# Performance work log

Measured on AMD Instinct MI355X. Metric: run time of the kernel, lower is better.

## Reference

```python
import jax, jax.numpy as jnp
import numpy as np

# Module constants (match init_kwargs)
H = 16            # num_heads
K = 64            # max_kernel_size
MAX_FREQ = 16.0
MIN_FREQ = 1.0
HALF_S = 16       # int(32**(1/1)) // 2
S = 2 * HALF_S + 1  # 33 sample offsets: -16..16
MAX_RECEPTIVE = HALF_S * MAX_FREQ  # 256.0


def setup_inputs() -> dict:
    key = jax.random.key(0)
    ks = jax.random.split(key, 6)
    B, L, C = 1, 4096, 1024
    x = jax.random.normal(ks[0], (B, L, C), dtype=jnp.float32)
    # Learned params (random small scale so offsets/kernels vary; torch inits
    # wave_proj to zeros but that degenerates the math under test).
    Ww = jax.random.normal(ks[1], (2 * H, C), dtype=jnp.float32) * 0.02
    bw = jnp.zeros((2 * H,), dtype=jnp.float32)
    Wk = jax.random.normal(ks[2], (H * K, C), dtype=jnp.float32) * 0.02
    bk = jnp.zeros((H * K,), dtype=jnp.float32)
    Wo = jax.random.normal(ks[3], (C, C), dtype=jnp.float32) * 0.02
    return {"x": x, "Ww": Ww, "bw": bw, "Wk": Wk, "bk": bk, "Wo": Wo}


def reference(x, Ww, bw, Wk, bk, Wo):
    B, L, C = x.shape
    D = C // H
    dt = x.dtype
    grid = jnp.arange(-HALF_S, HALF_S + 1, dtype=dt)  # (S,)

    # Predict per-position frequency / phase (averaged over heads)
    wp = jax.nn.silu(x @ Ww.T + bw).reshape(B, L, 2, H)
    freq = jax.nn.sigmoid(wp[:, :, 0]) * (MAX_FREQ - MIN_FREQ) + MIN_FREQ  # (B,L,H)
    phase = jnp.tanh(wp[:, :, 1]) * MAX_FREQ
    freq_avg = freq.mean(-1)    # (B,L)
    phase_avg = phase.mean(-1)  # (B,L)

    # Sample positions & gather indices
    rel_pos = grid[None, None, :] * freq_avg[..., None] + phase_avg[..., None]  # (B,L,S)
    centers = jnp.arange(L, dtype=dt)
    sample_pos = centers[None, :, None] + rel_pos                               # (B,L,S)
    valid = (sample_pos >= 0) & (sample_pos < L)
    sample_idx = jnp.clip(sample_pos.astype(jnp.int32), 0, L - 1)               # trunc toward 0, like torch .long()

    # Gather values: (B,L,S,C) -> (B,L,H,S,D)
    values = jax.vmap(lambda xf, idx: xf[idx])(x, sample_idx)
    values = values.reshape(B, L, S, H, D).transpose(0, 1, 3, 2, 4)

    # Kernel profile, linearly interpolated to sample positions
    kernel_max = jax.nn.silu(x @ Wk.T + bk).reshape(B, L, H, K)
    norm_pos = jnp.clip((rel_pos + MAX_RECEPTIVE) / (2.0 * MAX_RECEPTIVE), 0.0, 1.0)
    idx_float = norm_pos * (K - 1)                       # (B,L,S)
    idx_floor = jnp.clip(idx_float.astype(jnp.int32), 0, K - 2)
    w_ceil = (idx_float - idx_floor.astype(dt))[:, :, None, :]  # (B,L,1,S)
    w_floor = 1.0 - w_ceil
    ifl = jnp.broadcast_to(idx_floor[:, :, None, :], (B, L, H, S))
    k_floor = jnp.take_along_axis(kernel_max, ifl, axis=-1)
    k_ceil = jnp.take_along_axis(kernel_max, ifl + 1, axis=-1)
    kernel = (k_floor * w_floor + k_ceil * w_ceil) * valid[:, :, None, :].astype(dt)
    kernel = kernel / (kernel.sum(-1, keepdims=True) + 1e-8)

    out = jnp.einsum('blhsd,blhs->blhd', values, kernel).reshape(B, L, C)
    out = jax.nn.silu(out @ Wo.T)
    return out
```

## Files before the change

kernel.cpp:

```cpp
#include <hip/hip_runtime.h>
#include <math.h>

#define LDIM 4096
#define CDIM 1024
#define HDIM 16
#define KDIM 64
#define SDIM 33
#define HALF_SS 16
#define MAXF 16.0f
#define MINF 1.0f
#define MAXR 256.0f

__device__ __forceinline__ float sigmoid_np(float z) {
  float e = (float)exp(-(double)z);
  return __fdiv_rn(1.0f, __fadd_rn(1.0f, e));
}
__device__ __forceinline__ float silu_f(float z) {
  return __fmul_rn(z, sigmoid_np(z));
}

__device__ __forceinline__ float np_pairwise_sum(const float* a, int n) {
  float r[8];
#pragma unroll
  for (int j = 0; j < 8; ++j) r[j] = a[j];
  int i = 8;
  for (; i + 8 <= n; i += 8)
#pragma unroll
    for (int j = 0; j < 8; ++j) r[j] = __fadd_rn(r[j], a[i + j]);
  float res = __fadd_rn(__fadd_rn(__fadd_rn(r[0], r[1]), __fadd_rn(r[2], r[3])),
                        __fadd_rn(__fadd_rn(r[4], r[5]), __fadd_rn(r[6], r[7])));
  for (; i < n; ++i) res = __fadd_rn(res, a[i]);
  return res;
}

__global__ __launch_bounds__(256) void wave_kernel(
    const float* __restrict__ x, const float* __restrict__ Ww,
    const float* __restrict__ bw, float* __restrict__ fa, float* __restrict__ pa) {
  __shared__ float xs[CDIM];
  __shared__ float wp[2 * HDIM];
  int l = blockIdx.x;
  int tid = threadIdx.x;
  const float* xrow = x + (size_t)l * CDIM;
  for (int c = tid; c < CDIM; c += 256) xs[c] = xrow[c];
  __syncthreads();
  int j = tid >> 3, sub = tid & 7;
  const float* wrow = Ww + j * CDIM;
  double acc = 0.0;
  for (int c = sub; c < CDIM; c += 8) acc += (double)xs[c] * (double)wrow[c];
  for (int off = 4; off; off >>= 1) acc += __shfl_down(acc, off, 8);
  if (sub == 0) {
    float v32 = (float)(acc + (double)bw[j]);
    wp[j] = silu_f(v32);
  }
  __syncthreads();
  if (tid == 0) {
    float fv[HDIM], pv[HDIM];
    for (int h = 0; h < HDIM; ++h) {
      fv[h] = __fadd_rn(__fmul_rn(sigmoid_np(wp[h]), MAXF - MINF), MINF);
      float t32 = (float)tanh((double)wp[HDIM + h]);
      pv[h] = __fmul_rn(t32, MAXF);
    }
    fa[l] = __fdiv_rn(np_pairwise_sum(fv, HDIM), (float)HDIM);
    pa[l] = __fdiv_rn(np_pairwise_sum(pv, HDIM), (float)HDIM);
  }
}

__global__ __launch_bounds__(256) void gemm_bt_silu_f64(
    const float* __restrict__ A, const float* __restrict__ B,
    const float* __restrict__ bias, float* __restrict__ Cout,
    int M, int N, int Kd) {
  __shared__ double Asd[16][128];
  __shared__ double Bsd[16][64];
  int tid = threadIdx.x;
  int tx = tid & 15, ty = tid >> 4;
  int m0 = blockIdx.y * 128, n0 = blockIdx.x * 64;
  double acc[8][4] = {};
  for (int kt = 0; kt < Kd; kt += 16) {
#pragma unroll
    for (int q = 0; q < 2; ++q) {
      int e = tid + 256 * q;
      int row = e >> 2, kq = (e & 3) * 4;
      float4 va = *(const float4*)(A + (size_t)(m0 + row) * Kd + kt + kq);
      Asd[kq + 0][row] = (double)va.x; Asd[kq + 1][row] = (double)va.y;
      Asd[kq + 2][row] = (double)va.z; Asd[kq + 3][row] = (double)va.w;
    }
    {
      int row = tid >> 2, kq = (tid & 3) * 4;
      float4 vb = *(const float4*)(B + (size_t)(n0 + row) * Kd + kt + kq);
      Bsd[kq + 0][row] = (double)vb.x; Bsd[kq + 1][row] = (double)vb.y;
      Bsd[kq + 2][row] = (double)vb.z; Bsd[kq + 3][row] = (double)vb.w;
    }
    __syncthreads();
#pragma unroll
    for (int kk = 0; kk < 16; ++kk) {
      double a[8], b[4];
#pragma unroll
      for (int i = 0; i < 8; ++i) a[i] = Asd[kk][ty * 8 + i];
#pragma unroll
      for (int j2 = 0; j2 < 4; ++j2) b[j2] = Bsd[kk][tx * 4 + j2];
#pragma unroll
      for (int i = 0; i < 8; ++i)
#pragma unroll
        for (int j2 = 0; j2 < 4; ++j2) acc[i][j2] += a[i] * b[j2];
    }
    __syncthreads();
  }
#pragma unroll
  for (int i = 0; i < 8; ++i) {
    int mm = m0 + ty * 8 + i;
#pragma unroll
    for (int j2 = 0; j2 < 4; ++j2) {
      int nn = n0 + tx * 4 + j2;
      float v32 = (float)acc[i][j2];
      v32 = __fadd_rn(v32, bias[nn]);
      Cout[(size_t)mm * N + nn] = silu_f(v32);
    }
  }
}

__global__ __launch_bounds__(256) void gemm_bt_silu_f32(
    const float* __restrict__ A, const float* __restrict__ B,
    float* __restrict__ Cout, int M, int N, int Kd) {
  __shared__ float Asf[16][128];
  __shared__ float Bsf[16][128];
  int tid = threadIdx.x;
  int tx = tid & 15, ty = tid >> 4;
  int m0 = blockIdx.y * 128, n0 = blockIdx.x * 128;
  float acc[8][8] = {};
  for (int kt = 0; kt < Kd; kt += 16) {
#pragma unroll
    for (int q = 0; q < 2; ++q) {
      int e = tid + 256 * q;
      int row = e >> 2, kq = (e & 3) * 4;
      float4 va = *(const float4*)(A + (size_t)(m0 + row) * Kd + kt + kq);
      Asf[kq + 0][row] = va.x; Asf[kq + 1][row] = va.y;
      Asf[kq + 2][row] = va.z; Asf[kq + 3][row] = va.w;
      float4 vb = *(const float4*)(B + (size_t)(n0 + row) * Kd + kt + kq);
      Bsf[kq + 0][row] = vb.x; Bsf[kq + 1][row] = vb.y;
      Bsf[kq + 2][row] = vb.z; Bsf[kq + 3][row] = vb.w;
    }
    __syncthreads();
#pragma unroll
    for (int kk = 0; kk < 16; ++kk) {
      float4 a0 = *(const float4*)&Asf[kk][ty * 8];
      float4 a1 = *(const float4*)&Asf[kk][ty * 8 + 4];
      float4 b0 = *(const float4*)&Bsf[kk][tx * 8];
      float4 b1 = *(const float4*)&Bsf[kk][tx * 8 + 4];
      float a[8] = {a0.x, a0.y, a0.z, a0.w, a1.x, a1.y, a1.z, a1.w};
      float b[8] = {b0.x, b0.y, b0.z, b0.w, b1.x, b1.y, b1.z, b1.w};
#pragma unroll
      for (int i = 0; i < 8; ++i)
#pragma unroll
        for (int j2 = 0; j2 < 8; ++j2) acc[i][j2] += a[i] * b[j2];
    }
    __syncthreads();
  }
#pragma unroll
  for (int i = 0; i < 8; ++i) {
    int mm = m0 + ty * 8 + i;
#pragma unroll
    for (int j2 = 0; j2 < 8; ++j2) {
      int nn = n0 + tx * 8 + j2;
      Cout[(size_t)mm * N + nn] = silu_f(acc[i][j2]);
    }
  }
}

__global__ __launch_bounds__(256) void conv_kernel(
    const float* __restrict__ x, const float* __restrict__ km,
    const float* __restrict__ fa, const float* __restrict__ pa,
    float* __restrict__ conv) {
  int l = blockIdx.x;
  int tid = threadIdx.x;
  __shared__ int s_idx[SDIM];
  __shared__ int s_ifl[SDIM];
  __shared__ float s_wc[SDIM];
  __shared__ float s_val[SDIM];
  __shared__ float kern[HDIM][SDIM];
  __shared__ float s_den[HDIM];
  if (tid < SDIM) {
    float f = fa[l], p = pa[l];
    float rel = __fadd_rn(__fmul_rn((float)(tid - HALF_SS), f), p);
    float pos = __fadd_rn((float)l, rel);
    bool valid = (pos >= 0.f) && (pos < (float)LDIM);
    int idx = (int)pos;
    idx = min(max(idx, 0), LDIM - 1);
    s_idx[tid] = idx;
    s_val[tid] = valid ? 1.f : 0.f;
    float np_ = __fdiv_rn(__fadd_rn(rel, MAXR), 2.f * MAXR);
    np_ = fminf(fmaxf(np_, 0.f), 1.f);
    float idxf = __fmul_rn(np_, (float)(KDIM - 1));
    int ifl = (int)idxf;
    ifl = min(max(ifl, 0), KDIM - 2);
    s_ifl[tid] = ifl;
    s_wc[tid] = __fsub_rn(idxf, (float)ifl);
  }
  __syncthreads();
  for (int t = tid; t < HDIM * SDIM; t += 256) {
    int h = t / SDIM, s = t - h * SDIM;
    const float* kb = km + (size_t)l * CDIM + h * KDIM;
    float wc = s_wc[s];
    float wf = __fsub_rn(1.f, wc);
    float v = __fadd_rn(__fmul_rn(kb[s_ifl[s]], wf), __fmul_rn(kb[s_ifl[s] + 1], wc));
    kern[h][s] = __fmul_rn(v, s_val[s]);
  }
  __syncthreads();
  if (tid < HDIM) {
    float sum = np_pairwise_sum(&kern[tid][0], SDIM);
    s_den[tid] = __fadd_rn(sum, 1e-8f);
  }
  __syncthreads();
  for (int t = tid; t < HDIM * SDIM; t += 256) {
    int h = t / SDIM, s = t - h * SDIM;
    kern[h][s] = __fdiv_rn(kern[h][s], s_den[h]);
  }
  __syncthreads();
  float acc[4] = {0.f, 0.f, 0.f, 0.f};
  for (int s = 0; s < SDIM; ++s) {
    const float* xr = x + (size_t)s_idx[s] * CDIM;
#pragma unroll
    for (int q = 0; q < 4; ++q) {
      int c = tid + q * 256;
      acc[q] = __fadd_rn(acc[q], __fmul_rn(xr[c], kern[c >> 6][s]));
    }
  }
#pragma unroll
  for (int q = 0; q < 4; ++q) {
    int c = tid + q * 256;
    conv[(size_t)l * CDIM + c] = acc[q];
  }
}

extern "C" void kernel_launch(void* const* d_in, const int* in_sizes, int n_in,
                              void* d_out, int out_size, void* d_ws, size_t ws_size,
                              hipStream_t stream) {
  const float* x  = (const float*)d_in[0];
  const float* Ww = (const float*)d_in[1];
  const float* bw = (const float*)d_in[2];
  const float* Wk = (const float*)d_in[3];
  const float* bk = (const float*)d_in[4];
  const float* Wo = (const float*)d_in[5];
  float* out = (float*)d_out;

  float* fa   = (float*)d_ws;
  float* pa   = fa + LDIM;
  float* km   = pa + LDIM;
  float* conv = km + (size_t)LDIM * CDIM;

  wave_kernel<<<LDIM, 256, 0, stream>>>(x, Ww, bw, fa, pa);

  dim3 kmgrid(CDIM / 64, LDIM / 128);
  gemm_bt_silu_f64<<<kmgrid, 256, 0, stream>>>(x, Wk, bk, km, LDIM, CDIM, CDIM);

  conv_kernel<<<LDIM, 256, 0, stream>>>(x, km, fa, pa, conv);

  dim3 ogrid(CDIM / 128, LDIM / 128);
  gemm_bt_silu_f32<<<ogrid, 256, 0, stream>>>(conv, Wo, out, LDIM, CDIM, CDIM);
}
```

Baseline: 521.3 us.

## Replace fp64 kernel-profile GEMM with split-K fp32 GEMM plus reduce-silu pass

```diff
diff --git a/kernel.cpp b/kernel.cpp
--- a/kernel.cpp
+++ b/kernel.cpp
@@ -65,69 +65,19 @@
   }
 }
 
-__global__ __launch_bounds__(256) void gemm_bt_silu_f64(
+__global__ __launch_bounds__(256) void gemm_bt_ks2(
     const float* __restrict__ A, const float* __restrict__ B,
-    const float* __restrict__ bias, float* __restrict__ Cout,
+    float* __restrict__ P0, float* __restrict__ P1,
     int M, int N, int Kd) {
-  __shared__ double Asd[16][128];
-  __shared__ double Bsd[16][64];
-  int tid = threadIdx.x;
-  int tx = tid & 15, ty = tid >> 4;
-  int m0 = blockIdx.y * 128, n0 = blockIdx.x * 64;
-  double acc[8][4] = {};
-  for (int kt = 0; kt < Kd; kt += 16) {
-#pragma unroll
-    for (int q = 0; q < 2; ++q) {
-      int e = tid + 256 * q;
-      int row = e >> 2, kq = (e & 3) * 4;
-      float4 va = *(const float4*)(A + (size_t)(m0 + row) * Kd + kt + kq);
-      Asd[kq + 0][row] = (double)va.x; Asd[kq + 1][row] = (double)va.y;
-      Asd[kq + 2][row] = (double)va.z; Asd[kq + 3][row] = (double)va.w;
-    }
-    {
-      int row = tid >> 2, kq = (tid & 3) * 4;
-      float4 vb = *(const float4*)(B + (size_t)(n0 + row) * Kd + kt + kq);
-      Bsd[kq + 0][row] = (double)vb.x; Bsd[kq + 1][row] = (double)vb.y;
-      Bsd[kq + 2][row] = (double)vb.z; Bsd[kq + 3][row] = (double)vb.w;
-    }
-    __syncthreads();
-#pragma unroll
-    for (int kk = 0; kk < 16; ++kk) {
-      double a[8], b[4];
-#pragma unroll
-      for (int i = 0; i < 8; ++i) a[i] = Asd[kk][ty * 8 + i];
-#pragma unroll
-      for (int j2 = 0; j2 < 4; ++j2) b[j2] = Bsd[kk][tx * 4 + j2];
-#pragma unroll
-      for (int i = 0; i < 8; ++i)
-#pragma unroll
-        for (int j2 = 0; j2 < 4; ++j2) acc[i][j2] += a[i] * b[j2];
-    }
-    __syncthreads();
-  }
-#pragma unroll
-  for (int i = 0; i < 8; ++i) {
-    int mm = m0 + ty * 8 + i;
-#pragma unroll
-    for (int j2 = 0; j2 < 4; ++j2) {
-      int nn = n0 + tx * 4 + j2;
-      float v32 = (float)acc[i][j2];
-      v32 = __fadd_rn(v32, bias[nn]);
-      Cout[(size_t)mm * N + nn] = silu_f(v32);
-    }
-  }
-}
-
-__global__ __launch_bounds__(256) void gemm_bt_silu_f32(
-    const float* __restrict__ A, const float* __restrict__ B,
-    float* __restrict__ Cout, int M, int N, int Kd) {
-  __shared__ float Asf[16][128];
-  __shared__ float Bsf[16][128];
+  __shared__ float Asf[16][132];
+  __shared__ float Bsf[16][132];
   int tid = threadIdx.x;
   int tx = tid & 15, ty = tid >> 4;
   int m0 = blockIdx.y * 128, n0 = blockIdx.x * 128;
+  int k0 = blockIdx.z * (Kd >> 1), k1 = k0 + (Kd >> 1);
+  float* P = (blockIdx.z == 0) ? P0 : P1;
   float acc[8][8] = {};
-  for (int kt = 0; kt < Kd; kt += 16) {
+  for (int kt = k0; kt < k1; kt += 16) {
 #pragma unroll
     for (int q = 0; q < 2; ++q) {
       int e = tid + 256 * q;
@@ -158,19 +108,42 @@
 #pragma unroll
   for (int i = 0; i < 8; ++i) {
     int mm = m0 + ty * 8 + i;
-#pragma unroll
-    for (int j2 = 0; j2 < 8; ++j2) {
-      int nn = n0 + tx * 8 + j2;
-      Cout[(size_t)mm * N + nn] = silu_f(acc[i][j2]);
-    }
-  }
+    float4 o0 = {acc[i][0], acc[i][1], acc[i][2], acc[i][3]};
+    float4 o1 = {acc[i][4], acc[i][5], acc[i][6], acc[i][7]};
+    *(float4*)&P[(size_t)mm * N + n0 + tx * 8] = o0;
+    *(float4*)&P[(size_t)mm * N + n0 + tx * 8 + 4] = o1;
+  }
+}
+
+__global__ __launch_bounds__(256) void reduce_silu(
+    const float* __restrict__ p0, const float* __restrict__ p1,
+    const float* __restrict__ bias, float* __restrict__ o) {
+  int i = (blockIdx.x * 256 + threadIdx.x) * 4;
+  float4 a = *(const float4*)(p0 + i);
+  float4 b = *(const float4*)(p1 + i);
+  float4 r;
+  r.x = __fadd_rn(a.x, b.x);
+  r.y = __fadd_rn(a.y, b.y);
+  r.z = __fadd_rn(a.z, b.z);
+  r.w = __fadd_rn(a.w, b.w);
+  if (bias) {
+    int c = i & (CDIM - 1);
+    r.x = __fadd_rn(r.x, bias[c + 0]);
+    r.y = __fadd_rn(r.y, bias[c + 1]);
+    r.z = __fadd_rn(r.z, bias[c + 2]);
+    r.w = __fadd_rn(r.w, bias[c + 3]);
+  }
+  r.x = silu_f(r.x); r.y = silu_f(r.y);
+  r.z = silu_f(r.z); r.w = silu_f(r.w);
+  *(float4*)(o + i) = r;
 }
 
 __global__ __launch_bounds__(256) void conv_kernel(
     const float* __restrict__ x, const float* __restrict__ km,
     const float* __restrict__ fa, const float* __restrict__ pa,
     float* __restrict__ conv) {
-  int l = blockIdx.x;
+  int bid = blockIdx.x;
+  int l = (bid & 7) * (LDIM / 8) + (bid >> 3);
   int tid = threadIdx.x;
   __shared__ int s_idx[SDIM];
   __shared__ int s_ifl[SDIM];
@@ -215,20 +188,20 @@
     kern[h][s] = __fdiv_rn(kern[h][s], s_den[h]);
   }
   __syncthreads();
-  float acc[4] = {0.f, 0.f, 0.f, 0.f};
+  int c0 = tid * 4;
+  int h0 = c0 >> 6;
+  float acc0 = 0.f, acc1 = 0.f, acc2 = 0.f, acc3 = 0.f;
   for (int s = 0; s < SDIM; ++s) {
-    const float* xr = x + (size_t)s_idx[s] * CDIM;
-#pragma unroll
-    for (int q = 0; q < 4; ++q) {
-      int c = tid + q * 256;
-      acc[q] = __fadd_rn(acc[q], __fmul_rn(xr[c], kern[c >> 6][s]));
-    }
-  }
-#pragma unroll
-  for (int q = 0; q < 4; ++q) {
-    int c = tid + q * 256;
-    conv[(size_t)l * CDIM + c] = acc[q];
-  }
+    float4 xv = *(const float4*)(x + (size_t)s_idx[s] * CDIM + c0);
+    float kv = kern[h0][s];
+    acc0 = __fadd_rn(acc0, __fmul_rn(xv.x, kv));
+    acc1 = __fadd_rn(acc1, __fmul_rn(xv.y, kv));
+    acc2 = __fadd_rn(acc2, __fmul_rn(xv.z, kv));
+    acc3 = __fadd_rn(acc3, __fmul_rn(xv.w, kv));
+  }
+  float4 o;
+  o.x = acc0; o.y = acc1; o.z = acc2; o.w = acc3;
+  *(float4*)&conv[(size_t)l * CDIM + c0] = o;
 }
 
 extern "C" void kernel_launch(void* const* d_in, const int* in_sizes, int n_in,
@@ -249,11 +222,14 @@
 
   wave_kernel<<<LDIM, 256, 0, stream>>>(x, Ww, bw, fa, pa);
 
-  dim3 kmgrid(CDIM / 64, LDIM / 128);
-  gemm_bt_silu_f64<<<kmgrid, 256, 0, stream>>>(x, Wk, bk, km, LDIM, CDIM, CDIM);
+  dim3 ggrid(CDIM / 128, LDIM / 128, 2);
+  int rgrid = LDIM * CDIM / (4 * 256);
+
+  gemm_bt_ks2<<<ggrid, 256, 0, stream>>>(x, Wk, conv, out, LDIM, CDIM, CDIM);
+  reduce_silu<<<rgrid, 256, 0, stream>>>(conv, out, bk, km);
 
   conv_kernel<<<LDIM, 256, 0, stream>>>(x, km, fa, pa, conv);
 
-  dim3 ogrid(CDIM / 128, LDIM / 128);
-  gemm_bt_silu_f32<<<ogrid, 256, 0, stream>>>(conv, Wo, out, LDIM, CDIM, CDIM);
-}
+  gemm_bt_ks2<<<ggrid, 256, 0, stream>>>(conv, Wo, km, out, LDIM, CDIM, CDIM);
+  reduce_silu<<<rgrid, 256, 0, stream>>>(km, out, nullptr, out);
+}
```

New measurement: 417.4 us. 1.25x faster.
